# Kernel tuning notes

Hardware: AMD Instinct MI355X
Metric: run time of the kernel (lower is better)

The kernel has to match this reference:

```python
import jax, jax.numpy as jnp
import numpy as np

B, N, F_IN, HID, HEADS = 4, 10000, 128, 64, 4
E = 160000
NEG_SLOPE = 0.2


def _glorot(key, shape):
    fan_in, fan_out = shape[0], shape[-1]
    lim = jnp.sqrt(6.0 / (fan_in + fan_out)).astype(jnp.float32)
    return jax.random.uniform(key, shape, jnp.float32, -lim, lim)


def setup_inputs() -> dict:
    key = jax.random.key(0)
    ks = jax.random.split(key, 10)
    x = jax.random.normal(ks[0], (B, N, F_IN), jnp.float32)
    edge_index = jax.random.randint(ks[1], (2, E), 0, N, dtype=jnp.int32)
    return {
        "x": x,
        "edge_index": edge_index,
        "W1": _glorot(ks[2], (F_IN, HEADS * HID)),
        "a_src1": _glorot(ks[3], (HEADS, HID)),
        "a_dst1": _glorot(ks[4], (HEADS, HID)),
        "b1": jnp.zeros((HID,), jnp.float32),
        "W2": _glorot(ks[5], (HID, HEADS * HID)),
        "a_src2": _glorot(ks[6], (HEADS, HID)),
        "a_dst2": _glorot(ks[7], (HEADS, HID)),
        "b2": jnp.zeros((HID,), jnp.float32),
    }


def gat_conv(x, src, dst, W, a_src, a_dst, b):
    # x: [N, F]; src/dst: [E'] (self-loops already appended)
    h = (x @ W).reshape(N, HEADS, HID)              # [N, H, C]
    al_src = jnp.einsum("nhc,hc->nh", h, a_src)      # [N, H]
    al_dst = jnp.einsum("nhc,hc->nh", h, a_dst)
    e = jax.nn.leaky_relu(al_src[src] + al_dst[dst], NEG_SLOPE)  # [E', H]
    # segment softmax over incoming edges per destination node
    m = jax.ops.segment_max(e, dst, num_segments=N)  # [N, H]
    e = jnp.exp(e - m[dst])
    s = jax.ops.segment_sum(e, dst, num_segments=N)
    alpha = e / (s[dst] + 1e-16)                     # [E', H]
    out = jax.ops.segment_sum(alpha[:, :, None] * h[src], dst, num_segments=N)  # [N, H, C]
    return out.mean(axis=1) + b                      # concat=False -> head mean


def reference(x, edge_index, W1, a_src1, a_dst1, b1, W2, a_src2, a_dst2, b2):
    loops = jnp.arange(N, dtype=edge_index.dtype)
    src = jnp.concatenate([edge_index[0], loops])
    dst = jnp.concatenate([edge_index[1], loops])

    conv1 = jax.vmap(lambda xi: gat_conv(xi, src, dst, W1, a_src1, a_dst1, b1))
    conv2 = jax.vmap(lambda xi: gat_conv(xi, src, dst, W2, a_src2, a_dst2, b2))

    h = conv1(x)                 # [B, N, HID]
    h = jax.nn.elu(h)
    h = conv2(h)
    return h
```

## Files before the change

### kernel.cpp

```cpp
#include <hip/hip_runtime.h>
#include <hip/hip_fp16.h>
#include <math.h>

#define N_NODES 10000
#define B_BATCH 4
#define F_IN_C 128
#define HID_C 64
#define HEADS_C 4
#define E_EDGES 160000
#define E_TOT (E_EDGES + N_NODES)
#define E_PAD 200000
#define NEG_SLOPE 0.2f

typedef _Float16 half8 __attribute__((ext_vector_type(8)));
typedef float f32x4 __attribute__((ext_vector_type(4)));


__global__ void k_deg_init(int* __restrict__ deg) {
    int i = blockIdx.x * 256 + threadIdx.x;
    if (i < N_NODES) deg[i] = 1;
}

__global__ void k_deg_count(const int* __restrict__ ei, int* __restrict__ deg) {
    int e = blockIdx.x * 256 + threadIdx.x;
    if (e < E_EDGES) atomicAdd(&deg[ei[E_EDGES + e]], 1);
}

__global__ void k_scan(const int* __restrict__ deg, int* __restrict__ offs, int* __restrict__ cursor) {
    __shared__ int lds[1024];
    int t = threadIdx.x;
    int local[10];
    int tot = 0;
#pragma unroll
    for (int j = 0; j < 10; j++) {
        int i = t * 10 + j;
        int v = (i < N_NODES) ? ((deg[i] + 3) & ~3) : 0;
        tot += v;
        local[j] = tot;
    }
    lds[t] = tot;
    __syncthreads();
    for (int ofs = 1; ofs < 1024; ofs <<= 1) {
        int v = (t >= ofs) ? lds[t - ofs] : 0;
        __syncthreads();
        lds[t] += v;
        __syncthreads();
    }
    int base = lds[t] - tot;
#pragma unroll
    for (int j = 0; j < 10; j++) {
        int i = t * 10 + j;
        if (i < N_NODES) {
            offs[i + 1] = base + local[j];
            cursor[i] = (j == 0) ? base : base + local[j - 1];
        }
    }
    if (t == 0) offs[0] = 0;
}

__global__ void k_scatter(const int* __restrict__ ei, int* __restrict__ cursor,
                          int* __restrict__ csr_b, int* __restrict__ csr_dst) {
    int e = blockIdx.x * 256 + threadIdx.x;
    if (e < E_TOT) {
        int s, d;
        if (e < E_EDGES) { s = ei[e]; d = ei[E_EDGES + e]; }
        else { s = d = e - E_EDGES; }
        int pos = atomicAdd(&cursor[d], 1);
        csr_b[pos] = s << 7;
        csr_dst[pos] = d;
    }
}

__global__ void k_pad(const int* __restrict__ cursor, const int* __restrict__ offs,
                      int* __restrict__ csr_b, int* __restrict__ csr_dst) {
    int tid = blockIdx.x * 256 + threadIdx.x;
    if (tid >= N_NODES * 4) return;
    int d = tid >> 2, ps = tid & 3;
    int pos = cursor[d] + ps;
    if (pos < offs[d + 1]) { csr_b[pos] = 0; csr_dst[pos] = -1; }
}


template <int K>
__global__ void k_wext(const float* __restrict__ W, const float* __restrict__ asrc,
                       const float* __restrict__ adst, __half* __restrict__ Wt) {
    int tid = blockIdx.x * 256 + threadIdx.x;
    int nc = tid / K, k = tid % K;
    float v;
    if (nc < 256) {
        v = W[k * 256 + nc];
    } else if (nc < 260) {
        int hd = nc - 256; v = 0.f;
        for (int c = 0; c < 64; c++) v += W[k * 256 + hd * 64 + c] * asrc[hd * 64 + c];
    } else if (nc < 264) {
        int hd = nc - 260; v = 0.f;
        for (int c = 0; c < 64; c++) v += W[k * 256 + hd * 64 + c] * adst[hd * 64 + c];
    } else {
        v = 0.f;
    }
    Wt[(size_t)nc * K + k] = __float2half(v);
}


template <int K, typename XT>
__launch_bounds__(256)
__global__ void k_gemm(const XT* __restrict__ x, const __half* __restrict__ Wt,
                       __half* __restrict__ h2, float* __restrict__ alsrc, float* __restrict__ aldst) {
    int t = threadIdx.x;
    int w = t >> 6, lane = t & 63;
    int b = blockIdx.y;
    int node0 = blockIdx.x * 16;
    int col = lane & 15, kblk = lane >> 4;

    const XT* xr = x + ((size_t)b * N_NODES + node0 + col) * K + kblk * 8;

    f32x4 acc0 = {0.f, 0.f, 0.f, 0.f};
    f32x4 acc1 = {0.f, 0.f, 0.f, 0.f};
    f32x4 acc2 = {0.f, 0.f, 0.f, 0.f};
    f32x4 acc3 = {0.f, 0.f, 0.f, 0.f};
    f32x4 accal = {0.f, 0.f, 0.f, 0.f};

#pragma unroll
    for (int k0 = 0; k0 < K; k0 += 32) {
        half8 a;
        if constexpr (sizeof(XT) == 4) {
            float4 xa = *(const float4*)(xr + k0);
            float4 xc = *(const float4*)(xr + k0 + 4);
            a[0] = (_Float16)xa.x; a[1] = (_Float16)xa.y; a[2] = (_Float16)xa.z; a[3] = (_Float16)xa.w;
            a[4] = (_Float16)xc.x; a[5] = (_Float16)xc.y; a[6] = (_Float16)xc.z; a[7] = (_Float16)xc.w;
        } else {
            a = *(const half8*)(xr + k0);
        }
        const __half* wtk = Wt + kblk * 8 + k0;
        half8 b0 = *(const half8*)(wtk + (size_t)((w * 4 + 0) * 16 + col) * K);
        half8 b1 = *(const half8*)(wtk + (size_t)((w * 4 + 1) * 16 + col) * K);
        half8 b2 = *(const half8*)(wtk + (size_t)((w * 4 + 2) * 16 + col) * K);
        half8 b3 = *(const half8*)(wtk + (size_t)((w * 4 + 3) * 16 + col) * K);
        acc0 = __builtin_amdgcn_mfma_f32_16x16x32_f16(a, b0, acc0, 0, 0, 0);
        acc1 = __builtin_amdgcn_mfma_f32_16x16x32_f16(a, b1, acc1, 0, 0, 0);
        acc2 = __builtin_amdgcn_mfma_f32_16x16x32_f16(a, b2, acc2, 0, 0, 0);
        acc3 = __builtin_amdgcn_mfma_f32_16x16x32_f16(a, b3, acc3, 0, 0, 0);
        if (w == 0) {
            half8 bal = *(const half8*)(wtk + (size_t)(256 + col) * K);
            accal = __builtin_amdgcn_mfma_f32_16x16x32_f16(a, bal, accal, 0, 0, 0);
        }
    }

    {
        __half* dst = h2 + ((size_t)(b * 4 + w) * N_NODES + node0 + kblk * 4) * 64 + col;
#pragma unroll
        for (int r = 0; r < 4; r++) dst[(size_t)r * 64 + 0 * 16] = __float2half(acc0[r]);
#pragma unroll
        for (int r = 0; r < 4; r++) dst[(size_t)r * 64 + 1 * 16] = __float2half(acc1[r]);
#pragma unroll
        for (int r = 0; r < 4; r++) dst[(size_t)r * 64 + 2 * 16] = __float2half(acc2[r]);
#pragma unroll
        for (int r = 0; r < 4; r++) dst[(size_t)r * 64 + 3 * 16] = __float2half(acc3[r]);
    }
    if (w == 0 && col < 8) {
        int node = node0 + kblk * 4;
        size_t nb = (size_t)b * N_NODES;
        if (col < 4) {
            float* d = alsrc + (nb + node) * 4 + col;
#pragma unroll
            for (int r = 0; r < 4; r++) d[r * 4] = accal[r];
        } else {
            float* d = aldst + (nb + node) * 4 + (col - 4);
#pragma unroll
            for (int r = 0; r < 4; r++) d[r * 4] = accal[r];
        }
    }
}


__launch_bounds__(256)
__global__ void k_alpha(const float* __restrict__ alsrc, const float* __restrict__ aldst,
                        const int* __restrict__ csr_b, const int* __restrict__ csr_dst,
                        const int* __restrict__ offs, float* __restrict__ alpha) {
    int j = blockIdx.x * 256 + threadIdx.x;
    int e_act = offs[N_NODES];
    if (j >= e_act) return;
    int b = blockIdx.y;
    size_t base = (size_t)b * 4 * E_PAD + j;
    int dst = csr_dst[j];
    if (dst < 0) {
        alpha[base] = 0.f;
        alpha[base + E_PAD] = 0.f;
        alpha[base + (size_t)2 * E_PAD] = 0.f;
        alpha[base + (size_t)3 * E_PAD] = 0.f;
        return;
    }
    int src4 = csr_b[j] >> 5;
    const float* als = alsrc + (size_t)b * N_NODES * 4;
    float4 s4 = *(const float4*)(als + src4);
    float4 d4 = *(const float4*)(aldst + ((size_t)b * N_NODES + dst) * 4);
    float a;
    a = s4.x + d4.x; a = a > 0.f ? a : NEG_SLOPE * a; float e0 = __expf(a);
    a = s4.y + d4.y; a = a > 0.f ? a : NEG_SLOPE * a; float e1 = __expf(a);
    a = s4.z + d4.z; a = a > 0.f ? a : NEG_SLOPE * a; float e2 = __expf(a);
    a = s4.w + d4.w; a = a > 0.f ? a : NEG_SLOPE * a; float e3 = __expf(a);
    alpha[base] = e0;
    alpha[base + E_PAD] = e1;
    alpha[base + (size_t)2 * E_PAD] = e2;
    alpha[base + (size_t)3 * E_PAD] = e3;
}


#define QUAD_FMA16(p4, g0, g1, g2, g3)                                                    \
    {                                                                                     \
        float2 f01, f23;                                                                  \
        f01 = __half22float2(*(__half2*)&g0.x); f23 = __half22float2(*(__half2*)&g0.y);   \
        acc.x += p4.x * f01.x; acc.y += p4.x * f01.y; acc.z += p4.x * f23.x; acc.w += p4.x * f23.y; \
        f01 = __half22float2(*(__half2*)&g1.x); f23 = __half22float2(*(__half2*)&g1.y);   \
        acc.x += p4.y * f01.x; acc.y += p4.y * f01.y; acc.z += p4.y * f23.x; acc.w += p4.y * f23.y; \
        f01 = __half22float2(*(__half2*)&g2.x); f23 = __half22float2(*(__half2*)&g2.y);   \
        acc.x += p4.z * f01.x; acc.y += p4.z * f01.y; acc.z += p4.z * f23.x; acc.w += p4.z * f23.y; \
        f01 = __half22float2(*(__half2*)&g3.x); f23 = __half22float2(*(__half2*)&g3.y);   \
        acc.x += p4.w * f01.x; acc.y += p4.w * f01.y; acc.z += p4.w * f23.x; acc.w += p4.w * f23.y; \
        sacc += p4.x + p4.y + p4.z + p4.w;                                                \
    }

__launch_bounds__(256)
__global__ void k_agg(const __half* __restrict__ h2, const float* __restrict__ alpha,
                      const int* __restrict__ offs, const int* __restrict__ csr_b,
                      __half* __restrict__ oh) {
    int t = threadIdx.x;
    int bid = blockIdx.x;
    int combo = (bid & 7) + 8 * (bid / 5000);
    int local = (bid >> 3) % 625;
    int b = combo & 3, hd = combo >> 2;
    int wv = t >> 6, lane = t & 63;
    int grp = lane >> 4, cl = lane & 15;
    int dst = local * 16 + wv * 4 + grp;

    const char* hcb = (const char*)(h2 + (size_t)(b * 4 + hd) * N_NODES * 64);
    const float* ec = alpha + (size_t)(b * 4 + hd) * E_PAD;
    int s0 = offs[dst], s1 = offs[dst + 1];
    int cl8 = cl * 8;

    float4 acc = make_float4(0.f, 0.f, 0.f, 0.f);
    float sacc = 0.f;
    int4 c_cur = *(const int4*)(csr_b + s0);
    float4 p_cur = *(const float4*)(ec + s0);
    uint2 g0 = *(const uint2*)(hcb + (unsigned)(c_cur.x + cl8));
    uint2 g1 = *(const uint2*)(hcb + (unsigned)(c_cur.y + cl8));
    uint2 g2 = *(const uint2*)(hcb + (unsigned)(c_cur.z + cl8));
    uint2 g3 = *(const uint2*)(hcb + (unsigned)(c_cur.w + cl8));
    int jn = (s0 + 4 < s1) ? s0 + 4 : s0;
    int4 c_nxt = *(const int4*)(csr_b + jn);
    float4 p_nxt = *(const float4*)(ec + jn);

    for (int j = s0 + 4; j < s1; j += 4) {
        uint2 m0 = *(const uint2*)(hcb + (unsigned)(c_nxt.x + cl8));
        uint2 m1 = *(const uint2*)(hcb + (unsigned)(c_nxt.y + cl8));
        uint2 m2 = *(const uint2*)(hcb + (unsigned)(c_nxt.z + cl8));
        uint2 m3 = *(const uint2*)(hcb + (unsigned)(c_nxt.w + cl8));
        int j2 = (j + 4 < s1) ? j + 4 : j;
        int4 c_tmp = *(const int4*)(csr_b + j2);
        float4 p_tmp = *(const float4*)(ec + j2);
        QUAD_FMA16(p_cur, g0, g1, g2, g3)
        g0 = m0; g1 = m1; g2 = m2; g3 = m3;
        p_cur = p_nxt;
        c_nxt = c_tmp; p_nxt = p_tmp;
    }
    QUAD_FMA16(p_cur, g0, g1, g2, g3)

    float inv = 1.f / (sacc + 1e-16f);
    __half2 lo = __floats2half2_rn(acc.x * inv, acc.y * inv);
    __half2 hi = __floats2half2_rn(acc.z * inv, acc.w * inv);
    uint2 pk = make_uint2(*(unsigned*)&lo, *(unsigned*)&hi);
    *(uint2*)(oh + ((size_t)(b * 4 + hd) * N_NODES + dst) * 64 + cl * 4) = pk;
}


template <bool LAYER1>
__launch_bounds__(256)
__global__ void k_reduce(const __half* __restrict__ oh, const float* __restrict__ bias,
                         void* __restrict__ outv) {
    int tid = blockIdx.x * 256 + threadIdx.x;
    int c4 = (tid & 15) * 4;
    int n = (tid >> 4) % N_NODES;
    int b = tid / (N_NODES * 16);
    size_t base = ((size_t)(b * 4) * N_NODES + n) * 64 + c4;
    float4 s = make_float4(0.f, 0.f, 0.f, 0.f);
#pragma unroll
    for (int hd = 0; hd < 4; hd++) {
        uint2 v = *(const uint2*)(oh + base + (size_t)hd * N_NODES * 64);
        float2 f01 = __half22float2(*(__half2*)&v.x);
        float2 f23 = __half22float2(*(__half2*)&v.y);
        s.x += f01.x; s.y += f01.y; s.z += f23.x; s.w += f23.y;
    }
    float4 b4 = *(const float4*)(bias + c4);
    float ox = s.x * 0.25f + b4.x;
    float oy = s.y * 0.25f + b4.y;
    float oz = s.z * 0.25f + b4.z;
    float ow = s.w * 0.25f + b4.w;
    if (LAYER1) {
        ox = ox > 0.f ? ox : expm1f(ox);
        oy = oy > 0.f ? oy : expm1f(oy);
        oz = oz > 0.f ? oz : expm1f(oz);
        ow = ow > 0.f ? ow : expm1f(ow);
        __half2 lo = __floats2half2_rn(ox, oy);
        __half2 hi = __floats2half2_rn(oz, ow);
        uint2 pk = make_uint2(*(unsigned*)&lo, *(unsigned*)&hi);
        *(uint2*)((__half*)outv + ((size_t)b * N_NODES + n) * 64 + c4) = pk;
    } else {
        *(float4*)((float*)outv + ((size_t)b * N_NODES + n) * 64 + c4) = make_float4(ox, oy, oz, ow);
    }
}


extern "C" void kernel_launch(void* const* d_in, const int* in_sizes, int n_in,
                              void* d_out, int out_size, void* d_ws, size_t ws_size,
                              hipStream_t stream) {
    const float* x = (const float*)d_in[0];
    const int* ei = (const int*)d_in[1];
    const float* W1 = (const float*)d_in[2];
    const float* as1 = (const float*)d_in[3];
    const float* ad1 = (const float*)d_in[4];
    const float* b1 = (const float*)d_in[5];
    const float* W2 = (const float*)d_in[6];
    const float* as2 = (const float*)d_in[7];
    const float* ad2 = (const float*)d_in[8];
    const float* b2 = (const float*)d_in[9];
    float* out = (float*)d_out;

    char* p = (char*)d_ws;
    int* deg = (int*)p;            p += sizeof(int) * N_NODES;
    int* offs = (int*)p;           p += sizeof(int) * (N_NODES + 4);
    int* cursor = (int*)p;         p += sizeof(int) * N_NODES;
    int* csr_b = (int*)p;          p += sizeof(int) * E_PAD;
    int* csr_dst = (int*)p;        p += sizeof(int) * E_PAD;
    __half* Wt1 = (__half*)p;      p += sizeof(__half) * 272 * F_IN_C;
    __half* Wt2 = (__half*)p;      p += sizeof(__half) * 272 * HID_C;
    float* alsrc = (float*)p;      p += sizeof(float) * B_BATCH * N_NODES * 4;
    float* aldst = (float*)p;      p += sizeof(float) * B_BATCH * N_NODES * 4;
    __half* h2 = (__half*)p;       p += sizeof(__half) * (size_t)B_BATCH * N_NODES * 256;
    __half* oh = (__half*)p;       p += sizeof(__half) * (size_t)B_BATCH * N_NODES * 256;
    __half* x2 = (__half*)p;       p += sizeof(__half) * (size_t)B_BATCH * N_NODES * 64;
    p = (char*)(((size_t)p + 15) & ~(size_t)15);
    float* alpha = (float*)p;      p += sizeof(float) * (size_t)B_BATCH * 4 * E_PAD;

    k_wext<F_IN_C><<<272 * F_IN_C / 256, 256, 0, stream>>>(W1, as1, ad1, Wt1);
    k_wext<HID_C><<<272 * HID_C / 256, 256, 0, stream>>>(W2, as2, ad2, Wt2);

    k_deg_init<<<(N_NODES + 255) / 256, 256, 0, stream>>>(deg);
    k_deg_count<<<(E_EDGES + 255) / 256, 256, 0, stream>>>(ei, deg);
    k_scan<<<1, 1024, 0, stream>>>(deg, offs, cursor);
    k_scatter<<<(E_TOT + 255) / 256, 256, 0, stream>>>(ei, cursor, csr_b, csr_dst);
    k_pad<<<(N_NODES * 4 + 255) / 256, 256, 0, stream>>>(cursor, offs, csr_b, csr_dst);

    dim3 gGemm(N_NODES / 16, B_BATCH);
    dim3 gAlpha((E_PAD + 255) / 256, B_BATCH);
    int gAgg = 16 * 625;
    int gRed = B_BATCH * N_NODES * 16 / 256;

    k_gemm<F_IN_C, float><<<gGemm, 256, 0, stream>>>(x, Wt1, h2, alsrc, aldst);
    k_alpha<<<gAlpha, 256, 0, stream>>>(alsrc, aldst, csr_b, csr_dst, offs, alpha);
    k_agg<<<gAgg, 256, 0, stream>>>(h2, alpha, offs, csr_b, oh);
    k_reduce<true><<<gRed, 256, 0, stream>>>(oh, b1, x2);

    k_gemm<HID_C, __half><<<gGemm, 256, 0, stream>>>(x2, Wt2, h2, alsrc, aldst);
    k_alpha<<<gAlpha, 256, 0, stream>>>(alsrc, aldst, csr_b, csr_dst, offs, alpha);
    k_agg<<<gAgg, 256, 0, stream>>>(h2, alpha, offs, csr_b, oh);
    k_reduce<false><<<gRed, 256, 0, stream>>>(oh, b2, out);
}
```

Baseline: 220.6 us.

## Fuse head-mean reduction into aggregation and merge setup kernels

The aggregation kernel now assigns one destination node per wavefront, with the four 16-lane groups covering the four heads. The head mean is done in-register with cross-lane shuffles, followed by bias and ELU, which removes the separate reduce kernel and the oh intermediate buffer. The weight-extension and degree-init kernels are merged into one setup launch to cut launch count. Lanes in a wave now walk different heads with the same edge count, so load balance across dst nodes changes per wave.

```diff
diff --git a/kernel.cpp b/kernel.cpp
--- a/kernel.cpp
+++ b/kernel.cpp
@@ -16,75 +16,9 @@
 typedef float f32x4 __attribute__((ext_vector_type(4)));
 
 
-__global__ void k_deg_init(int* __restrict__ deg) {
-    int i = blockIdx.x * 256 + threadIdx.x;
-    if (i < N_NODES) deg[i] = 1;
-}
-
-__global__ void k_deg_count(const int* __restrict__ ei, int* __restrict__ deg) {
-    int e = blockIdx.x * 256 + threadIdx.x;
-    if (e < E_EDGES) atomicAdd(&deg[ei[E_EDGES + e]], 1);
-}
-
-__global__ void k_scan(const int* __restrict__ deg, int* __restrict__ offs, int* __restrict__ cursor) {
-    __shared__ int lds[1024];
-    int t = threadIdx.x;
-    int local[10];
-    int tot = 0;
-#pragma unroll
-    for (int j = 0; j < 10; j++) {
-        int i = t * 10 + j;
-        int v = (i < N_NODES) ? ((deg[i] + 3) & ~3) : 0;
-        tot += v;
-        local[j] = tot;
-    }
-    lds[t] = tot;
-    __syncthreads();
-    for (int ofs = 1; ofs < 1024; ofs <<= 1) {
-        int v = (t >= ofs) ? lds[t - ofs] : 0;
-        __syncthreads();
-        lds[t] += v;
-        __syncthreads();
-    }
-    int base = lds[t] - tot;
-#pragma unroll
-    for (int j = 0; j < 10; j++) {
-        int i = t * 10 + j;
-        if (i < N_NODES) {
-            offs[i + 1] = base + local[j];
-            cursor[i] = (j == 0) ? base : base + local[j - 1];
-        }
-    }
-    if (t == 0) offs[0] = 0;
-}
-
-__global__ void k_scatter(const int* __restrict__ ei, int* __restrict__ cursor,
-                          int* __restrict__ csr_b, int* __restrict__ csr_dst) {
-    int e = blockIdx.x * 256 + threadIdx.x;
-    if (e < E_TOT) {
-        int s, d;
-        if (e < E_EDGES) { s = ei[e]; d = ei[E_EDGES + e]; }
-        else { s = d = e - E_EDGES; }
-        int pos = atomicAdd(&cursor[d], 1);
-        csr_b[pos] = s << 7;
-        csr_dst[pos] = d;
-    }
-}
-
-__global__ void k_pad(const int* __restrict__ cursor, const int* __restrict__ offs,
-                      int* __restrict__ csr_b, int* __restrict__ csr_dst) {
-    int tid = blockIdx.x * 256 + threadIdx.x;
-    if (tid >= N_NODES * 4) return;
-    int d = tid >> 2, ps = tid & 3;
-    int pos = cursor[d] + ps;
-    if (pos < offs[d + 1]) { csr_b[pos] = 0; csr_dst[pos] = -1; }
-}
-
-
-template <int K>
-__global__ void k_wext(const float* __restrict__ W, const float* __restrict__ asrc,
-                       const float* __restrict__ adst, __half* __restrict__ Wt) {
-    int tid = blockIdx.x * 256 + threadIdx.x;
+__device__ void wext_body(const float* __restrict__ W, const float* __restrict__ asrc,
+                          const float* __restrict__ adst, __half* __restrict__ Wt,
+                          int tid, int K) {
     int nc = tid / K, k = tid % K;
     float v;
     if (nc < 256) {
@@ -99,6 +33,82 @@
         v = 0.f;
     }
     Wt[(size_t)nc * K + k] = __float2half(v);
+}
+
+__global__ void k_setup(const float* __restrict__ W1, const float* __restrict__ as1,
+                        const float* __restrict__ ad1, const float* __restrict__ W2,
+                        const float* __restrict__ as2, const float* __restrict__ ad2,
+                        __half* __restrict__ Wt1, __half* __restrict__ Wt2,
+                        int* __restrict__ deg) {
+    int blk = blockIdx.x;
+    if (blk < 136) {
+        wext_body(W1, as1, ad1, Wt1, blk * 256 + threadIdx.x, F_IN_C);
+    } else if (blk < 204) {
+        wext_body(W2, as2, ad2, Wt2, (blk - 136) * 256 + threadIdx.x, HID_C);
+    } else {
+        int i = (blk - 204) * 256 + threadIdx.x;
+        if (i < N_NODES) deg[i] = 1;
+    }
+}
+
+
+__global__ void k_deg_count(const int* __restrict__ ei, int* __restrict__ deg) {
+    int e = blockIdx.x * 256 + threadIdx.x;
+    if (e < E_EDGES) atomicAdd(&deg[ei[E_EDGES + e]], 1);
+}
+
+__global__ void k_scan(const int* __restrict__ deg, int* __restrict__ offs, int* __restrict__ cursor) {
+    __shared__ int lds[1024];
+    int t = threadIdx.x;
+    int local[10];
+    int tot = 0;
+#pragma unroll
+    for (int j = 0; j < 10; j++) {
+        int i = t * 10 + j;
+        int v = (i < N_NODES) ? ((deg[i] + 3) & ~3) : 0;
+        tot += v;
+        local[j] = tot;
+    }
+    lds[t] = tot;
+    __syncthreads();
+    for (int ofs = 1; ofs < 1024; ofs <<= 1) {
+        int v = (t >= ofs) ? lds[t - ofs] : 0;
+        __syncthreads();
+        lds[t] += v;
+        __syncthreads();
+    }
+    int base = lds[t] - tot;
+#pragma unroll
+    for (int j = 0; j < 10; j++) {
+        int i = t * 10 + j;
+        if (i < N_NODES) {
+            offs[i + 1] = base + local[j];
+            cursor[i] = (j == 0) ? base : base + local[j - 1];
+        }
+    }
+    if (t == 0) offs[0] = 0;
+}
+
+__global__ void k_scatter(const int* __restrict__ ei, int* __restrict__ cursor,
+                          int* __restrict__ csr_b, int* __restrict__ csr_dst) {
+    int e = blockIdx.x * 256 + threadIdx.x;
+    if (e < E_TOT) {
+        int s, d;
+        if (e < E_EDGES) { s = ei[e]; d = ei[E_EDGES + e]; }
+        else { s = d = e - E_EDGES; }
+        int pos = atomicAdd(&cursor[d], 1);
+        csr_b[pos] = s << 7;
+        csr_dst[pos] = d;
+    }
+}
+
+__global__ void k_pad(const int* __restrict__ cursor, const int* __restrict__ offs,
+                      int* __restrict__ csr_b, int* __restrict__ csr_dst) {
+    int tid = blockIdx.x * 256 + threadIdx.x;
+    if (tid >= N_NODES * 4) return;
+    int d = tid >> 2, ps = tid & 3;
+    int pos = cursor[d] + ps;
+    if (pos < offs[d + 1]) { csr_b[pos] = 0; csr_dst[pos] = -1; }
 }
 
 
@@ -220,18 +230,19 @@
         sacc += p4.x + p4.y + p4.z + p4.w;                                                \
     }
 
+template <bool LAYER1>
 __launch_bounds__(256)
 __global__ void k_agg(const __half* __restrict__ h2, const float* __restrict__ alpha,
                       const int* __restrict__ offs, const int* __restrict__ csr_b,
-                      __half* __restrict__ oh) {
+                      const float* __restrict__ bias, void* __restrict__ outv) {
     int t = threadIdx.x;
     int bid = blockIdx.x;
-    int combo = (bid & 7) + 8 * (bid / 5000);
-    int local = (bid >> 3) % 625;
-    int b = combo & 3, hd = combo >> 2;
+    int xcd = bid & 7;
+    int b = xcd >> 1;
+    int local = (bid >> 3) * 2 + (xcd & 1);
     int wv = t >> 6, lane = t & 63;
-    int grp = lane >> 4, cl = lane & 15;
-    int dst = local * 16 + wv * 4 + grp;
+    int hd = lane >> 4, cl = lane & 15;
+    int dst = local * 4 + wv;
 
     const char* hcb = (const char*)(h2 + (size_t)(b * 4 + hd) * N_NODES * 64);
     const float* ec = alpha + (size_t)(b * 4 + hd) * E_PAD;
@@ -266,46 +277,33 @@
     QUAD_FMA16(p_cur, g0, g1, g2, g3)
 
     float inv = 1.f / (sacc + 1e-16f);
-    __half2 lo = __floats2half2_rn(acc.x * inv, acc.y * inv);
-    __half2 hi = __floats2half2_rn(acc.z * inv, acc.w * inv);
-    uint2 pk = make_uint2(*(unsigned*)&lo, *(unsigned*)&hi);
-    *(uint2*)(oh + ((size_t)(b * 4 + hd) * N_NODES + dst) * 64 + cl * 4) = pk;
-}
-
-
-template <bool LAYER1>
-__launch_bounds__(256)
-__global__ void k_reduce(const __half* __restrict__ oh, const float* __restrict__ bias,
-                         void* __restrict__ outv) {
-    int tid = blockIdx.x * 256 + threadIdx.x;
-    int c4 = (tid & 15) * 4;
-    int n = (tid >> 4) % N_NODES;
-    int b = tid / (N_NODES * 16);
-    size_t base = ((size_t)(b * 4) * N_NODES + n) * 64 + c4;
-    float4 s = make_float4(0.f, 0.f, 0.f, 0.f);
-#pragma unroll
-    for (int hd = 0; hd < 4; hd++) {
-        uint2 v = *(const uint2*)(oh + base + (size_t)hd * N_NODES * 64);
-        float2 f01 = __half22float2(*(__half2*)&v.x);
-        float2 f23 = __half22float2(*(__half2*)&v.y);
-        s.x += f01.x; s.y += f01.y; s.z += f23.x; s.w += f23.y;
-    }
-    float4 b4 = *(const float4*)(bias + c4);
-    float ox = s.x * 0.25f + b4.x;
-    float oy = s.y * 0.25f + b4.y;
-    float oz = s.z * 0.25f + b4.z;
-    float ow = s.w * 0.25f + b4.w;
-    if (LAYER1) {
-        ox = ox > 0.f ? ox : expm1f(ox);
-        oy = oy > 0.f ? oy : expm1f(oy);
-        oz = oz > 0.f ? oz : expm1f(oz);
-        ow = ow > 0.f ? ow : expm1f(ow);
-        __half2 lo = __floats2half2_rn(ox, oy);
-        __half2 hi = __floats2half2_rn(oz, ow);
-        uint2 pk = make_uint2(*(unsigned*)&lo, *(unsigned*)&hi);
-        *(uint2*)((__half*)outv + ((size_t)b * N_NODES + n) * 64 + c4) = pk;
-    } else {
-        *(float4*)((float*)outv + ((size_t)b * N_NODES + n) * 64 + c4) = make_float4(ox, oy, oz, ow);
+    float4 v = make_float4(acc.x * inv, acc.y * inv, acc.z * inv, acc.w * inv);
+#pragma unroll
+    for (int o = 16; o < 64; o <<= 1) {
+        v.x += __shfl_xor(v.x, o);
+        v.y += __shfl_xor(v.y, o);
+        v.z += __shfl_xor(v.z, o);
+        v.w += __shfl_xor(v.w, o);
+    }
+    if (lane < 16) {
+        float4 b4 = *(const float4*)(bias + cl * 4);
+        float ox = v.x * 0.25f + b4.x;
+        float oy = v.y * 0.25f + b4.y;
+        float oz = v.z * 0.25f + b4.z;
+        float ow = v.w * 0.25f + b4.w;
+        if (LAYER1) {
+            ox = ox > 0.f ? ox : expm1f(ox);
+            oy = oy > 0.f ? oy : expm1f(oy);
+            oz = oz > 0.f ? oz : expm1f(oz);
+            ow = ow > 0.f ? ow : expm1f(ow);
+            __half2 lo = __floats2half2_rn(ox, oy);
+            __half2 hi = __floats2half2_rn(oz, ow);
+            uint2 pk = make_uint2(*(unsigned*)&lo, *(unsigned*)&hi);
+            *(uint2*)((__half*)outv + ((size_t)b * N_NODES + dst) * 64 + cl * 4) = pk;
+        } else {
+            *(float4*)((float*)outv + ((size_t)b * N_NODES + dst) * 64 + cl * 4) =
+                make_float4(ox, oy, oz, ow);
+        }
     }
 }
 
@@ -336,15 +334,12 @@
     float* alsrc = (float*)p;      p += sizeof(float) * B_BATCH * N_NODES * 4;
     float* aldst = (float*)p;      p += sizeof(float) * B_BATCH * N_NODES * 4;
     __half* h2 = (__half*)p;       p += sizeof(__half) * (size_t)B_BATCH * N_NODES * 256;
-    __half* oh = (__half*)p;       p += sizeof(__half) * (size_t)B_BATCH * N_NODES * 256;
     __half* x2 = (__half*)p;       p += sizeof(__half) * (size_t)B_BATCH * N_NODES * 64;
     p = (char*)(((size_t)p + 15) & ~(size_t)15);
     float* alpha = (float*)p;      p += sizeof(float) * (size_t)B_BATCH * 4 * E_PAD;
 
-    k_wext<F_IN_C><<<272 * F_IN_C / 256, 256, 0, stream>>>(W1, as1, ad1, Wt1);
-    k_wext<HID_C><<<272 * HID_C / 256, 256, 0, stream>>>(W2, as2, ad2, Wt2);
-
-    k_deg_init<<<(N_NODES + 255) / 256, 256, 0, stream>>>(deg);
+    k_setup<<<244, 256, 0, stream>>>(W1, as1, ad1, W2, as2, ad2, Wt1, Wt2, deg);
+
     k_deg_count<<<(E_EDGES + 255) / 256, 256, 0, stream>>>(ei, deg);
     k_scan<<<1, 1024, 0, stream>>>(deg, offs, cursor);
     k_scatter<<<(E_TOT + 255) / 256, 256, 0, stream>>>(ei, cursor, csr_b, csr_dst);
@@ -352,16 +347,13 @@
 
     dim3 gGemm(N_NODES / 16, B_BATCH);
     dim3 gAlpha((E_PAD + 255) / 256, B_BATCH);
-    int gAgg = 16 * 625;
-    int gRed = B_BATCH * N_NODES * 16 / 256;
+    int gAgg = B_BATCH * 2500;
 
     k_gemm<F_IN_C, float><<<gGemm, 256, 0, stream>>>(x, Wt1, h2, alsrc, aldst);
     k_alpha<<<gAlpha, 256, 0, stream>>>(alsrc, aldst, csr_b, csr_dst, offs, alpha);
-    k_agg<<<gAgg, 256, 0, stream>>>(h2, alpha, offs, csr_b, oh);
-    k_reduce<true><<<gRed, 256, 0, stream>>>(oh, b1, x2);
+    k_agg<true><<<gAgg, 256, 0, stream>>>(h2, alpha, offs, csr_b, b1, x2);
 
     k_gemm<HID_C, __half><<<gGemm, 256, 0, stream>>>(x2, Wt2, h2, alsrc, aldst);
     k_alpha<<<gAlpha, 256, 0, stream>>>(alsrc, aldst, csr_b, csr_dst, offs, alpha);
-    k_agg<<<gAgg, 256, 0, stream>>>(h2, alpha, offs, csr_b, oh);
-    k_reduce<false><<<gRed, 256, 0, stream>>>(oh, b2, out);
-}
+    k_agg<false><<<gAgg, 256, 0, stream>>>(h2, alpha, offs, csr_b, b2, out);
+}
```

Measured after the change: 207.6 us. 1.06x faster.
